# Kernel optimization log

Measured on AMD Instinct MI355X. Metric: run time of the kernel, lower is better.

Reference implementation:

```python
import jax, jax.numpy as jnp
import numpy as np
from jax import lax

NC = 8  # num_classes
NUM_ITERS = 2


def _resize_bilinear_ac(x, out_h, out_w):
    """Bilinear resize with align_corners=True, x: (N, C, H, W)."""
    N, C, H, W = x.shape

    def coords(n_out, n_in):
        if n_out == 1:
            return jnp.zeros((1,), jnp.float32)
        return jnp.linspace(0.0, float(n_in - 1), n_out, dtype=jnp.float32)

    ys = coords(out_h, H)
    xs = coords(out_w, W)
    y0 = jnp.floor(ys).astype(jnp.int32)
    y1 = jnp.minimum(y0 + 1, H - 1)
    wy = (ys - y0.astype(jnp.float32)).astype(x.dtype)
    x0 = jnp.floor(xs).astype(jnp.int32)
    x1 = jnp.minimum(x0 + 1, W - 1)
    wx = (xs - x0.astype(jnp.float32)).astype(x.dtype)

    r0 = x[:, :, y0, :]
    r1 = x[:, :, y1, :]
    r = r0 * (1.0 - wy)[None, None, :, None] + r1 * wy[None, None, :, None]
    c0 = r[:, :, :, x0]
    c1 = r[:, :, :, x1]
    return c0 * (1.0 - wx)[None, None, None, :] + c1 * wx[None, None, None, :]


def _conv2d(x, w, groups=1):
    k = w.shape[-1]
    pad = k // 2
    return lax.conv_general_dilated(
        x, w, window_strides=(1, 1), padding=[(pad, pad), (pad, pad)],
        dimension_numbers=('NCHW', 'OIHW', 'NCHW'), feature_group_count=groups)


def _mean_field_update(unary, guidance, spatial_w, bilateral_w, compat_w):
    Q = jax.nn.softmax(unary, axis=1)
    cw = compat_w[:, :, 0, 0]  # (O, I)
    for _ in range(NUM_ITERS):
        spatial_msg = _conv2d(Q, spatial_w, groups=NC)          # depthwise 3x3
        bilateral_in = jnp.concatenate([Q, guidance], axis=1)   # (N, NC+6, H, W)
        bilateral_msg = _conv2d(bilateral_in, bilateral_w)      # 3x3 dense
        message = spatial_msg + bilateral_msg
        message = jnp.einsum('nchw,oc->nohw', message, cw)      # 1x1 compat conv
        Q = jax.nn.softmax(unary - message, axis=1)
    return Q


def setup_inputs() -> dict:
    key = jax.random.key(0)
    ks = jax.random.split(key, 16)
    inp = {
        'logits': jax.random.normal(ks[0], (8, NC, 512, 512), jnp.float32),
        'image': jax.random.uniform(ks[1], (8, 3, 512, 512), jnp.float32),
        'skip0': jax.random.normal(ks[2], (8, 64, 256, 256), jnp.float32),
        'skip1': jax.random.normal(ks[3], (8, 128, 128, 128), jnp.float32),
        'skip2': jax.random.normal(ks[4], (8, 256, 64, 64), jnp.float32),
        'skip3': jax.random.normal(ks[5], (8, 512, 32, 32), jnp.float32),
        'spatial_w': jax.random.normal(ks[6], (NC, 1, 3, 3), jnp.float32) * 0.1,
        'bilateral_w': jax.random.normal(ks[7], (NC, NC + 6, 3, 3), jnp.float32) * 0.1,
        # compat_conv is initialized to -I (zeros then -= eye) in the module
        'compat_w': (-jnp.eye(NC, dtype=jnp.float32)).reshape(NC, NC, 1, 1),
        'skip_w0': jax.random.normal(ks[8], (3, 64, 1, 1), jnp.float32) * 0.05,
        'skip_b0': jnp.zeros((3,), jnp.float32),
        'skip_w1': jax.random.normal(ks[9], (3, 128, 1, 1), jnp.float32) * 0.05,
        'skip_b1': jnp.zeros((3,), jnp.float32),
        'skip_w2': jax.random.normal(ks[10], (3, 256, 1, 1), jnp.float32) * 0.05,
        'skip_b2': jnp.zeros((3,), jnp.float32),
        'skip_w3': jax.random.normal(ks[11], (3, 512, 1, 1), jnp.float32) * 0.05,
        'skip_b3': jnp.zeros((3,), jnp.float32),
    }
    return inp


def reference(logits, image, skip0, skip1, skip2, skip3,
              spatial_w, bilateral_w, compat_w,
              skip_w0, skip_b0, skip_w1, skip_b1,
              skip_w2, skip_b2, skip_w3, skip_b3):
    H, W = logits.shape[2], logits.shape[3]

    # fuse_skip_features: 1x1 project each skip to 3ch, upsample, average
    skips = [skip0, skip1, skip2, skip3]
    ws = [skip_w0, skip_w1, skip_w2, skip_w3]
    bs = [skip_b0, skip_b1, skip_b2, skip_b3]
    fused = jnp.zeros((logits.shape[0], 3, H, W), logits.dtype)
    for feat, w, b in zip(skips, ws, bs):
        p = jnp.einsum('nchw,oc->nohw', feat, w[:, :, 0, 0]) + b[None, :, None, None]
        fused = fused + _resize_bilinear_ac(p, H, W)
    fused = fused / len(skips)

    guidance = jnp.concatenate([image, fused], axis=1)  # (N, 6, H, W)

    Q_full = _mean_field_update(logits, guidance, spatial_w, bilateral_w, compat_w)

    logits_down = _resize_bilinear_ac(logits, H // 2, W // 2)
    guidance_down = _resize_bilinear_ac(guidance, H // 2, W // 2)
    Q_down = _mean_field_update(logits_down, guidance_down, spatial_w, bilateral_w, compat_w)
    Q_down_up = _resize_bilinear_ac(Q_down, H, W)

    return (Q_full + Q_down_up) / 2.0
```

## Files before the change

kernel.cpp:

```cpp
#include <hip/hip_runtime.h>
#include <hip/hip_fp16.h>
#include <math.h>

#define NB 8
#define NCLS 8
#define NGU 6
#define NBI 14
#define HF 512
#define WF 512
#define HH 256
#define WH 256

#define TOX 32
#define TOY 16
#define SX 36
#define SY 20
#define SPX (SY * SX)
#define R1W 36
#define R1N (18 * 36)
#define R1T 41
#define R2T 32
#define PLANE (SPX * 8)
#define PSTR (PLANE + 32)
#define TILEH (16 + PSTR + PLANE + 16)

typedef _Float16 f16x8 __attribute__((ext_vector_type(8)));
typedef float f32x4 __attribute__((ext_vector_type(4)));

static __device__ __forceinline__ void ac_prep(int o, float scale, int insz,
                                               int& i0, int& i1, float& f) {
    float s = (float)o * scale;
    int ii = (int)floorf(s);
    if (ii > insz - 1) ii = insz - 1;
    if (ii < 0) ii = 0;
    i0 = ii;
    i1 = (ii + 1 < insz) ? (ii + 1) : (insz - 1);
    f = s - (float)ii;
}

__global__ void k_fill_bias(float* __restrict__ out, const float* __restrict__ b, int HW) {
    int total = NB * 3 * HW;
    int idx = blockIdx.x * blockDim.x + threadIdx.x;
    if (idx >= total) return;
    int o = (idx / HW) % 3;
    out[idx] = b[o];
}

template <int VEC, bool DIRECT>
__global__ void k_skip_proj(const float* __restrict__ feat, const float* __restrict__ w,
                            const float* __restrict__ bias, float* __restrict__ out,
                            int C, int HW, int nch) {
    __shared__ float sw[3 * 512];
    for (int i = threadIdx.x; i < 3 * C; i += blockDim.x) sw[i] = w[i];
    __syncthreads();
    const int HWv = HW / VEC;
    int total = NB * HWv * nch;
    for (int idx = blockIdx.x * blockDim.x + threadIdx.x; idx < total;
         idx += gridDim.x * blockDim.x) {
        int hv = idx % HWv;
        int t = idx / HWv;
        int ch = t % nch;
        int n = t / nch;
        int c0 = ch * 64;
        const float* fp = feat + ((size_t)n * C + c0) * HW + (size_t)hv * VEC;
        float a[3][VEC];
        #pragma unroll
        for (int o = 0; o < 3; ++o)
            #pragma unroll
            for (int k = 0; k < VEC; ++k) a[o][k] = 0.f;
        #pragma unroll 4
        for (int c = 0; c < 64; ++c) {
            float v[VEC];
            if constexpr (VEC == 4) {
                float4 t4 = *reinterpret_cast<const float4*>(fp + (size_t)c * HW);
                v[0] = t4.x; v[1] = t4.y; v[2] = t4.z; v[3] = t4.w;
            } else if constexpr (VEC == 2) {
                float2 t2 = *reinterpret_cast<const float2*>(fp + (size_t)c * HW);
                v[0] = t2.x; v[1] = t2.y;
            } else {
                v[0] = fp[(size_t)c * HW];
            }
            #pragma unroll
            for (int o = 0; o < 3; ++o) {
                const float wv = sw[o * C + c0 + c];
                #pragma unroll
                for (int k = 0; k < VEC; ++k) a[o][k] = fmaf(wv, v[k], a[o][k]);
            }
        }
        float* op = out + (size_t)n * 3 * HW + (size_t)hv * VEC;
        #pragma unroll
        for (int o = 0; o < 3; ++o) {
            #pragma unroll
            for (int k = 0; k < VEC; ++k) {
                if (DIRECT)
                    op[(size_t)o * HW + k] = bias[o] + a[o][k];
                else
                    atomicAdd(&op[(size_t)o * HW + k], a[o][k]);
            }
        }
    }
}

__global__ void k_prep_full(const float* __restrict__ logits, const float* __restrict__ image,
                            const float* __restrict__ p0, const float* __restrict__ p1,
                            const float* __restrict__ p2, const float* __restrict__ p3,
                            _Float16* __restrict__ Gh, _Float16* __restrict__ Q0h) {
    const int HW = HF * WF;
    int idx = blockIdx.x * blockDim.x + threadIdx.x;
    if (idx >= NB * HW) return;
    int n = idx / HW, r = idx - n * HW;
    int y = r / WF, x = r - y * WF;

    const float* ps[4] = {p0, p1, p2, p3};
    const int ss[4] = {256, 128, 64, 32};
    float f[3] = {0.f, 0.f, 0.f};
    #pragma unroll
    for (int l = 0; l < 4; ++l) {
        int s = ss[l];
        float scale = (float)(s - 1) / 511.0f;
        int y0, y1, x0, x1;
        float fy, fx;
        ac_prep(y, scale, s, y0, y1, fy);
        ac_prep(x, scale, s, x0, x1, fx);
        const float* pb = ps[l] + (size_t)n * 3 * s * s;
        #pragma unroll
        for (int o = 0; o < 3; ++o) {
            const float* pp = pb + (size_t)o * s * s;
            float v00 = pp[y0 * s + x0], v01 = pp[y0 * s + x1];
            float v10 = pp[y1 * s + x0], v11 = pp[y1 * s + x1];
            float r0 = v00 * (1.f - fy) + v10 * fy;
            float r1 = v01 * (1.f - fy) + v11 * fy;
            f[o] += r0 * (1.f - fx) + r1 * fx;
        }
    }
    const float* ip = image + (size_t)n * 3 * HW + r;
    f16x8 gv;
    #pragma unroll
    for (int o = 0; o < 3; ++o) gv[o] = (_Float16)ip[(size_t)o * HW];
    #pragma unroll
    for (int o = 0; o < 3; ++o) gv[3 + o] = (_Float16)(f[o] * 0.25f);
    gv[6] = (_Float16)0.f;
    gv[7] = (_Float16)0.f;
    *(f16x8*)(Gh + (size_t)idx * 8) = gv;

    const float* up = logits + (size_t)n * NCLS * HW + r;
    float e[8];
    float s = 0.f;
    #pragma unroll
    for (int o = 0; o < 8; ++o) { e[o] = __expf(up[(size_t)o * HW]); s += e[o]; }
    float inv = 1.f / s;
    f16x8 qv;
    #pragma unroll
    for (int o = 0; o < 8; ++o) qv[o] = (_Float16)(e[o] * inv);
    *(f16x8*)(Q0h + (size_t)idx * 8) = qv;
}

__global__ void k_prep_w(const float* __restrict__ wsp, const float* __restrict__ wbil,
                         const float* __restrict__ cw, float* __restrict__ W2) {
    int i = blockIdx.x * blockDim.x + threadIdx.x;
    if (i >= NBI * 9 * 8) return;
    int o = i & 7;
    int t = (i >> 3) % 9;
    int ci = i / 72;
    float s = 0.f;
    for (int c = 0; c < NCLS; ++c)
        s += cw[o * NCLS + c] * wbil[((size_t)c * NBI + ci) * 9 + t];
    if (ci < NCLS) s += cw[o * NCLS + ci] * wsp[ci * 9 + t];
    W2[ci * 72 + t * 8 + o] = s;
}

__global__ void k_prep_frag(const float* __restrict__ W2, _Float16* __restrict__ wf) {
    int i = blockIdx.x * blockDim.x + threadIdx.x;
    if (i >= 5 * 64) return;
    int j = i >> 6, l = i & 63;
    int col = l & 15, kg = l >> 4;
    #pragma unroll
    for (int e = 0; e < 8; ++e) {
        int k = j * 32 + kg * 8 + e;
        int tap = k >> 4, ci = k & 15;
        float v = (tap < 9 && ci < 14 && col < 8) ? W2[ci * 72 + tap * 8 + col] : 0.f;
        wf[i * 8 + e] = (_Float16)v;
    }
}

template <bool DOWN, bool UPFOLD>
__global__ __launch_bounds__(256, 4) void k_mf_mfma(
    const float* __restrict__ unary, const _Float16* __restrict__ Q0h,
    const _Float16* __restrict__ Gh, const _Float16* __restrict__ Qd,
    void* __restrict__ QoutV, const _Float16* __restrict__ wfragG,
    int H, int W, int Hs, int Ws) {
    __shared__ __align__(16) _Float16 s_t[TILEH];
    __shared__ __align__(16) _Float16 s_msg[R1N * 8];
    _Float16* tb0 = s_t + 16;
    _Float16* tb1 = s_t + 16 + PSTR;

    const int tid = threadIdx.x;
    const int lane = tid & 63;
    const int wv = tid >> 6;
    const int n = blockIdx.z;
    const int gx0 = blockIdx.x * TOX;
    const int gy0 = blockIdx.y * TOY;
    const int HW = H * W;
    const int HWs = Hs * Ws;

    f16x8 wf[5];
    #pragma unroll
    for (int j = 0; j < 5; ++j)
        wf[j] = *(const f16x8*)(wfragG + (j * 64 + lane) * 8);

    if (tid < 16) s_t[tid] = (_Float16)0.f;
    else if (tid < 48) s_t[5760 + tid] = (_Float16)0.f;
    else if (tid < 64) s_t[11520 + tid] = (_Float16)0.f;

    const float syc = DOWN ? (float)(Hs - 1) / (float)(H - 1) : 1.f;
    const float sxc = DOWN ? (float)(Ws - 1) / (float)(W - 1) : 1.f;
    for (int i = tid; i < SPX; i += 256) {
        int yy = i / SX, xx = i - yy * SX;
        int gy = gy0 + yy - 2, gx = gx0 + xx - 2;
        f16x8 qv, gv;
        #pragma unroll
        for (int o = 0; o < 8; ++o) { qv[o] = (_Float16)0.f; gv[o] = (_Float16)0.f; }
        if ((unsigned)gy < (unsigned)H && (unsigned)gx < (unsigned)W) {
            if (DOWN) {
                int y0, y1, x0, x1;
                float fy, fx;
                ac_prep(gy, syc, Hs, y0, y1, fy);
                ac_prep(gx, sxc, Ws, x0, x1, fx);
                const float w00 = (1.f - fy) * (1.f - fx), w01 = (1.f - fy) * fx;
                const float w10 = fy * (1.f - fx), w11 = fy * fx;
                const size_t o00 = (size_t)y0 * Ws + x0, o01 = (size_t)y0 * Ws + x1;
                const size_t o10 = (size_t)y1 * Ws + x0, o11 = (size_t)y1 * Ws + x1;
                const float* ubase = unary + (size_t)n * NCLS * HWs;
                float e[8];
                float s = 0.f;
                #pragma unroll
                for (int o = 0; o < 8; ++o) {
                    const float* up = ubase + (size_t)o * HWs;
                    float u = w00 * up[o00] + w01 * up[o01] + w10 * up[o10] + w11 * up[o11];
                    e[o] = __expf(u);
                    s += e[o];
                }
                float inv = 1.f / s;
                #pragma unroll
                for (int o = 0; o < 8; ++o) qv[o] = (_Float16)(e[o] * inv);
                const size_t gb = (size_t)n * HWs;
                f16x8 ga = *(const f16x8*)(Gh + (gb + o00) * 8);
                f16x8 gb2 = *(const f16x8*)(Gh + (gb + o01) * 8);
                f16x8 gc = *(const f16x8*)(Gh + (gb + o10) * 8);
                f16x8 gd = *(const f16x8*)(Gh + (gb + o11) * 8);
                #pragma unroll
                for (int c = 0; c < 8; ++c) {
                    float g = w00 * (float)ga[c] + w01 * (float)gb2[c] +
                              w10 * (float)gc[c] + w11 * (float)gd[c];
                    gv[c] = (_Float16)g;
                }
            } else {
                const size_t off = ((size_t)n * HW + (size_t)gy * W + gx) * 8;
                qv = *(const f16x8*)(Q0h + off);
                gv = *(const f16x8*)(Gh + off);
            }
        }
        *(f16x8*)(tb0 + i * 8) = qv;
        *(f16x8*)(tb1 + i * 8) = gv;
    }
    __syncthreads();

    for (int t = wv; t < R1T; t += 4) {
        int pb = t * 16;
        int p = pb + (lane & 15);
        if (p > R1N - 1) p = R1N - 1;
        int qy = p / R1W;
        int yy = 1 + qy, xx = p - qy * R1W;
        int kg = lane >> 4;
        f32x4 acc = {0.f, 0.f, 0.f, 0.f};
        #pragma unroll
        for (int j = 0; j < 5; ++j) {
            int tap = 2 * j + (kg >> 1);
            if (tap > 8) tap = 8;
            int dy = tap / 3 - 1, dx = tap - (tap / 3) * 3 - 1;
            int idx = (yy + dy) * SX + (xx + dx);
            f16x8 af = *(const f16x8*)(tb0 + (kg & 1) * PSTR + idx * 8);
            acc = __builtin_amdgcn_mfma_f32_16x16x32_f16(af, wf[j], acc, 0, 0, 0);
        }
        int ch = lane & 15;
        if (ch < 8) {
            int pxb = pb + (lane >> 4) * 4;
            #pragma unroll
            for (int r = 0; r < 4; ++r) {
                int px = pxb + r;
                if (px < R1N) s_msg[px * 8 + ch] = (_Float16)acc[r];
            }
        }
    }
    __syncthreads();

    for (int i = tid; i < R1N; i += 256) {
        int qy = i / R1W;
        int yy = 1 + qy, xx = i - qy * R1W;
        int gy = gy0 + yy - 2, gx = gx0 + xx - 2;
        if ((unsigned)gy < (unsigned)H && (unsigned)gx < (unsigned)W) {
            f16x8 m = *(const f16x8*)(s_msg + i * 8);
            f16x8 q0 = *(const f16x8*)(tb0 + (i + SX) * 8);
            float e[8];
            float s = 0.f;
            #pragma unroll
            for (int o = 0; o < 8; ++o) {
                e[o] = (float)q0[o] * __expf(-(float)m[o]);
                s += e[o];
            }
            float inv = 1.f / s;
            f16x8 q1;
            #pragma unroll
            for (int o = 0; o < 8; ++o) q1[o] = (_Float16)(e[o] * inv);
            *(f16x8*)(tb0 + (i + SX) * 8) = q1;
        }
    }
    f16x8 m1r[2];
    #pragma unroll
    for (int u2 = 0; u2 < 2; ++u2) {
        int i = tid + 256 * u2;
        int oy = i >> 5, ox = i & 31;
        int r1 = (1 + oy) * R1W + (2 + ox);
        m1r[u2] = *(const f16x8*)(s_msg + r1 * 8);
    }
    __syncthreads();

    for (int t = wv; t < R2T; t += 4) {
        int pb = t * 16;
        int p = pb + (lane & 15);
        int yy = 2 + (p >> 5), xx = 2 + (p & 31);
        int kg = lane >> 4;
        f32x4 acc = {0.f, 0.f, 0.f, 0.f};
        #pragma unroll
        for (int j = 0; j < 5; ++j) {
            int tap = 2 * j + (kg >> 1);
            if (tap > 8) tap = 8;
            int dy = tap / 3 - 1, dx = tap - (tap / 3) * 3 - 1;
            int idx = (yy + dy) * SX + (xx + dx);
            f16x8 af = *(const f16x8*)(tb0 + (kg & 1) * PSTR + idx * 8);
            acc = __builtin_amdgcn_mfma_f32_16x16x32_f16(af, wf[j], acc, 0, 0, 0);
        }
        int ch = lane & 15;
        if (ch < 8) {
            int pxb = pb + (lane >> 4) * 4;
            #pragma unroll
            for (int r = 0; r < 4; ++r) s_msg[(pxb + r) * 8 + ch] = (_Float16)acc[r];
        }
    }
    __syncthreads();

    #pragma unroll
    for (int u2 = 0; u2 < 2; ++u2) {
        int i = tid + 256 * u2;
        int oy = i >> 5, ox = i & 31;
        int gy = gy0 + oy, gx = gx0 + ox;
        f16x8 m2 = *(const f16x8*)(s_msg + i * 8);
        f16x8 q1 = *(const f16x8*)(tb0 + ((2 + oy) * SX + (2 + ox)) * 8);
        float e[8];
        float s = 0.f;
        #pragma unroll
        for (int o = 0; o < 8; ++o) {
            e[o] = (float)q1[o] * __expf((float)m1r[u2][o] - (float)m2[o]);
            s += e[o];
        }
        float inv = 1.f / s;
        if (UPFOLD) {
            float* qp = (float*)QoutV + (size_t)n * NCLS * HW + (size_t)gy * W + gx;
            int y0, y1, x0, x1;
            float fy, fx;
            ac_prep(gy, 255.f / 511.f, HH, y0, y1, fy);
            ac_prep(gx, 255.f / 511.f, WH, x0, x1, fx);
            const float w00 = (1.f - fy) * (1.f - fx), w01 = (1.f - fy) * fx;
            const float w10 = fy * (1.f - fx), w11 = fy * fx;
            const size_t qb = (size_t)n * (HH * WH);
            f16x8 qa = *(const f16x8*)(Qd + (qb + (size_t)y0 * WH + x0) * 8);
            f16x8 qbv = *(const f16x8*)(Qd + (qb + (size_t)y0 * WH + x1) * 8);
            f16x8 qc = *(const f16x8*)(Qd + (qb + (size_t)y1 * WH + x0) * 8);
            f16x8 qdv = *(const f16x8*)(Qd + (qb + (size_t)y1 * WH + x1) * 8);
            #pragma unroll
            for (int o = 0; o < 8; ++o) {
                float v = w00 * (float)qa[o] + w01 * (float)qbv[o] +
                          w10 * (float)qc[o] + w11 * (float)qdv[o];
                qp[(size_t)o * HW] = fmaf(0.5f, e[o] * inv, 0.5f * v);
            }
        } else {
            _Float16* qo = (_Float16*)QoutV + ((size_t)n * HW + (size_t)gy * W + gx) * 8;
            f16x8 q2;
            #pragma unroll
            for (int o = 0; o < 8; ++o) q2[o] = (_Float16)(e[o] * inv);
            *(f16x8*)qo = q2;
        }
    }
}

static inline int cdiv(int a, int b) { return (a + b - 1) / b; }

extern "C" void kernel_launch(void* const* d_in, const int* in_sizes, int n_in,
                              void* d_out, int out_size, void* d_ws, size_t ws_size,
                              hipStream_t stream) {
    const float* logits = (const float*)d_in[0];
    const float* image = (const float*)d_in[1];
    const float* skip0 = (const float*)d_in[2];
    const float* skip1 = (const float*)d_in[3];
    const float* skip2 = (const float*)d_in[4];
    const float* skip3 = (const float*)d_in[5];
    const float* spatial_w = (const float*)d_in[6];
    const float* bilateral_w = (const float*)d_in[7];
    const float* compat_w = (const float*)d_in[8];
    const float* skip_w0 = (const float*)d_in[9];
    const float* skip_b0 = (const float*)d_in[10];
    const float* skip_w1 = (const float*)d_in[11];
    const float* skip_b1 = (const float*)d_in[12];
    const float* skip_w2 = (const float*)d_in[13];
    const float* skip_b2 = (const float*)d_in[14];
    const float* skip_w3 = (const float*)d_in[15];
    const float* skip_b3 = (const float*)d_in[16];
    float* out = (float*)d_out;
    float* ws = (float*)d_ws;

    float* p0 = ws + 0;
    float* p1 = ws + 1572864;
    float* p2 = ws + 1966080;
    float* p3 = ws + 2064384;
    float* W2 = ws + 2100000;
    _Float16* wfrag = (_Float16*)(ws + 2110000);
    _Float16* Q0h = (_Float16*)(ws + 4194304);
    _Float16* Gh = (_Float16*)(ws + 12582912);
    _Float16* Qdh = (_Float16*)(ws + 20971520);

    const int HWf = HF * WF;

    k_prep_w<<<4, 256, 0, stream>>>(spatial_w, bilateral_w, compat_w, W2);
    k_prep_frag<<<2, 256, 0, stream>>>(W2, wfrag);

    k_fill_bias<<<cdiv(NB * 3 * 16384, 256), 256, 0, stream>>>(p1, skip_b1, 16384);
    k_fill_bias<<<cdiv(NB * 3 * 4096, 256), 256, 0, stream>>>(p2, skip_b2, 4096);
    k_fill_bias<<<cdiv(NB * 3 * 1024, 256), 256, 0, stream>>>(p3, skip_b3, 1024);

    k_skip_proj<4, true><<<cdiv(NB * 16384 * 1, 256), 256, 0, stream>>>(
        skip0, skip_w0, skip_b0, p0, 64, 65536, 1);
    k_skip_proj<4, false><<<cdiv(NB * 4096 * 2, 256), 256, 0, stream>>>(
        skip1, skip_w1, skip_b1, p1, 128, 16384, 2);
    k_skip_proj<2, false><<<cdiv(NB * 2048 * 4, 256), 256, 0, stream>>>(
        skip2, skip_w2, skip_b2, p2, 256, 4096, 4);
    k_skip_proj<1, false><<<cdiv(NB * 1024 * 8, 256), 256, 0, stream>>>(
        skip3, skip_w3, skip_b3, p3, 512, 1024, 8);

    k_prep_full<<<cdiv(NB * HWf, 256), 256, 0, stream>>>(logits, image, p0, p1, p2, p3, Gh, Q0h);

    {
        dim3 grid(WH / TOX, HH / TOY, NB);
        k_mf_mfma<true, false><<<grid, 256, 0, stream>>>(
            logits, nullptr, Gh, nullptr, (void*)Qdh, wfrag, HH, WH, HF, WF);
    }

    {
        dim3 grid(WF / TOX, HF / TOY, NB);
        k_mf_mfma<false, true><<<grid, 256, 0, stream>>>(
            nullptr, Q0h, Gh, Qdh, (void*)out, wfrag, HF, WF, HF, WF);
    }
}
```

Before: 230.6 us.

## Merge prep launches, vectorize prep_full by two pixels, DMA interior tiles to LDS

Merges the two weight-prep kernels into one single-block kernel and the three bias-fill kernels into one, cutting launch count. k_prep_full now handles two adjacent pixels per thread with float2 loads of image and logits. For interior tiles of the full-resolution mean-field kernel, the Q0/guidance halo is copied with global_load_lds DMA straight into shared memory, and the bounds check in the softmax step is skipped there. The DMA path relies on the halo rows mapping contiguously to LDS, and relies on the existing barrier to cover completion of the async loads.

```diff
diff --git a/kernel.cpp b/kernel.cpp
--- a/kernel.cpp
+++ b/kernel.cpp
@@ -38,12 +38,21 @@
     f = s - (float)ii;
 }
 
-__global__ void k_fill_bias(float* __restrict__ out, const float* __restrict__ b, int HW) {
-    int total = NB * 3 * HW;
-    int idx = blockIdx.x * blockDim.x + threadIdx.x;
-    if (idx >= total) return;
-    int o = (idx / HW) % 3;
-    out[idx] = b[o];
+static __device__ __forceinline__ void dma16(const _Float16* g, _Float16* l) {
+    __builtin_amdgcn_global_load_lds(
+        (const __attribute__((address_space(1))) void*)g,
+        (__attribute__((address_space(3))) void*)l, 16, 0, 0);
+}
+
+__global__ void k_fill3(float* __restrict__ p1, float* __restrict__ p2,
+                        float* __restrict__ p3, const float* __restrict__ b1,
+                        const float* __restrict__ b2, const float* __restrict__ b3) {
+    int i = blockIdx.x * blockDim.x + threadIdx.x;
+    if (i < NB * 3 * 16384) { p1[i] = b1[(i / 16384) % 3]; return; }
+    i -= NB * 3 * 16384;
+    if (i < NB * 3 * 4096) { p2[i] = b2[(i / 4096) % 3]; return; }
+    i -= NB * 3 * 4096;
+    if (i < NB * 3 * 1024) p3[i] = b3[(i / 1024) % 3];
 }
 
 template <int VEC, bool DIRECT>
@@ -106,80 +115,98 @@
                             const float* __restrict__ p2, const float* __restrict__ p3,
                             _Float16* __restrict__ Gh, _Float16* __restrict__ Q0h) {
     const int HW = HF * WF;
-    int idx = blockIdx.x * blockDim.x + threadIdx.x;
-    if (idx >= NB * HW) return;
+    int t = blockIdx.x * blockDim.x + threadIdx.x;
+    if (t >= NB * HW / 2) return;
+    int idx = t * 2;
     int n = idx / HW, r = idx - n * HW;
     int y = r / WF, x = r - y * WF;
 
     const float* ps[4] = {p0, p1, p2, p3};
     const int ss[4] = {256, 128, 64, 32};
-    float f[3] = {0.f, 0.f, 0.f};
+    float f[2][3] = {{0.f, 0.f, 0.f}, {0.f, 0.f, 0.f}};
     #pragma unroll
     for (int l = 0; l < 4; ++l) {
         int s = ss[l];
         float scale = (float)(s - 1) / 511.0f;
-        int y0, y1, x0, x1;
-        float fy, fx;
+        int y0, y1;
+        float fy;
         ac_prep(y, scale, s, y0, y1, fy);
-        ac_prep(x, scale, s, x0, x1, fx);
         const float* pb = ps[l] + (size_t)n * 3 * s * s;
         #pragma unroll
-        for (int o = 0; o < 3; ++o) {
-            const float* pp = pb + (size_t)o * s * s;
-            float v00 = pp[y0 * s + x0], v01 = pp[y0 * s + x1];
-            float v10 = pp[y1 * s + x0], v11 = pp[y1 * s + x1];
-            float r0 = v00 * (1.f - fy) + v10 * fy;
-            float r1 = v01 * (1.f - fy) + v11 * fy;
-            f[o] += r0 * (1.f - fx) + r1 * fx;
+        for (int k = 0; k < 2; ++k) {
+            int x0, x1;
+            float fx;
+            ac_prep(x + k, scale, s, x0, x1, fx);
+            #pragma unroll
+            for (int o = 0; o < 3; ++o) {
+                const float* pp = pb + (size_t)o * s * s;
+                float v00 = pp[y0 * s + x0], v01 = pp[y0 * s + x1];
+                float v10 = pp[y1 * s + x0], v11 = pp[y1 * s + x1];
+                float r0 = v00 * (1.f - fy) + v10 * fy;
+                float r1 = v01 * (1.f - fy) + v11 * fy;
+                f[k][o] += r0 * (1.f - fx) + r1 * fx;
+            }
         }
     }
     const float* ip = image + (size_t)n * 3 * HW + r;
-    f16x8 gv;
-    #pragma unroll
-    for (int o = 0; o < 3; ++o) gv[o] = (_Float16)ip[(size_t)o * HW];
-    #pragma unroll
-    for (int o = 0; o < 3; ++o) gv[3 + o] = (_Float16)(f[o] * 0.25f);
-    gv[6] = (_Float16)0.f;
-    gv[7] = (_Float16)0.f;
-    *(f16x8*)(Gh + (size_t)idx * 8) = gv;
-
+    float2 img[3];
+    #pragma unroll
+    for (int o = 0; o < 3; ++o) img[o] = *reinterpret_cast<const float2*>(&ip[(size_t)o * HW]);
     const float* up = logits + (size_t)n * NCLS * HW + r;
-    float e[8];
-    float s = 0.f;
-    #pragma unroll
-    for (int o = 0; o < 8; ++o) { e[o] = __expf(up[(size_t)o * HW]); s += e[o]; }
-    float inv = 1.f / s;
-    f16x8 qv;
-    #pragma unroll
-    for (int o = 0; o < 8; ++o) qv[o] = (_Float16)(e[o] * inv);
-    *(f16x8*)(Q0h + (size_t)idx * 8) = qv;
-}
-
-__global__ void k_prep_w(const float* __restrict__ wsp, const float* __restrict__ wbil,
-                         const float* __restrict__ cw, float* __restrict__ W2) {
-    int i = blockIdx.x * blockDim.x + threadIdx.x;
-    if (i >= NBI * 9 * 8) return;
-    int o = i & 7;
-    int t = (i >> 3) % 9;
-    int ci = i / 72;
-    float s = 0.f;
-    for (int c = 0; c < NCLS; ++c)
-        s += cw[o * NCLS + c] * wbil[((size_t)c * NBI + ci) * 9 + t];
-    if (ci < NCLS) s += cw[o * NCLS + ci] * wsp[ci * 9 + t];
-    W2[ci * 72 + t * 8 + o] = s;
-}
-
-__global__ void k_prep_frag(const float* __restrict__ W2, _Float16* __restrict__ wf) {
-    int i = blockIdx.x * blockDim.x + threadIdx.x;
-    if (i >= 5 * 64) return;
-    int j = i >> 6, l = i & 63;
-    int col = l & 15, kg = l >> 4;
-    #pragma unroll
-    for (int e = 0; e < 8; ++e) {
-        int k = j * 32 + kg * 8 + e;
-        int tap = k >> 4, ci = k & 15;
-        float v = (tap < 9 && ci < 14 && col < 8) ? W2[ci * 72 + tap * 8 + col] : 0.f;
-        wf[i * 8 + e] = (_Float16)v;
+    float2 u[8];
+    #pragma unroll
+    for (int o = 0; o < 8; ++o) u[o] = *reinterpret_cast<const float2*>(&up[(size_t)o * HW]);
+
+    f16x8 gv[2], qv[2];
+    #pragma unroll
+    for (int k = 0; k < 2; ++k) {
+        gv[k][0] = (_Float16)(k ? img[0].y : img[0].x);
+        gv[k][1] = (_Float16)(k ? img[1].y : img[1].x);
+        gv[k][2] = (_Float16)(k ? img[2].y : img[2].x);
+        gv[k][3] = (_Float16)(f[k][0] * 0.25f);
+        gv[k][4] = (_Float16)(f[k][1] * 0.25f);
+        gv[k][5] = (_Float16)(f[k][2] * 0.25f);
+        gv[k][6] = (_Float16)0.f;
+        gv[k][7] = (_Float16)0.f;
+        float e[8];
+        float s = 0.f;
+        #pragma unroll
+        for (int o = 0; o < 8; ++o) { e[o] = __expf(k ? u[o].y : u[o].x); s += e[o]; }
+        float inv = 1.f / s;
+        #pragma unroll
+        for (int o = 0; o < 8; ++o) qv[k][o] = (_Float16)(e[o] * inv);
+    }
+    *(f16x8*)(Gh + (size_t)idx * 8) = gv[0];
+    *(f16x8*)(Gh + (size_t)idx * 8 + 8) = gv[1];
+    *(f16x8*)(Q0h + (size_t)idx * 8) = qv[0];
+    *(f16x8*)(Q0h + (size_t)idx * 8 + 8) = qv[1];
+}
+
+__global__ void k_prep_wf(const float* __restrict__ wsp, const float* __restrict__ wbil,
+                          const float* __restrict__ cw, _Float16* __restrict__ wf) {
+    __shared__ float sW2[NBI * 72];
+    int tid = threadIdx.x;
+    if (tid < NBI * 72) {
+        int o = tid & 7;
+        int t = (tid >> 3) % 9;
+        int ci = tid / 72;
+        float s = 0.f;
+        for (int c = 0; c < NCLS; ++c)
+            s += cw[o * NCLS + c] * wbil[((size_t)c * NBI + ci) * 9 + t];
+        if (ci < NCLS) s += cw[o * NCLS + ci] * wsp[ci * 9 + t];
+        sW2[tid] = s;
+    }
+    __syncthreads();
+    if (tid < 5 * 64) {
+        int l = tid & 63;
+        int col = l & 15, kg = l >> 4;
+        #pragma unroll
+        for (int e = 0; e < 8; ++e) {
+            int k = (tid >> 6) * 32 + kg * 8 + e;
+            int tap = k >> 4, ci = k & 15;
+            float v = (tap < 9 && ci < 14 && col < 8) ? sW2[ci * 72 + tap * 8 + col] : 0.f;
+            wf[tid * 8 + e] = (_Float16)v;
+        }
     }
 }
 
@@ -212,56 +239,72 @@
     else if (tid < 48) s_t[5760 + tid] = (_Float16)0.f;
     else if (tid < 64) s_t[11520 + tid] = (_Float16)0.f;
 
-    const float syc = DOWN ? (float)(Hs - 1) / (float)(H - 1) : 1.f;
-    const float sxc = DOWN ? (float)(Ws - 1) / (float)(W - 1) : 1.f;
-    for (int i = tid; i < SPX; i += 256) {
-        int yy = i / SX, xx = i - yy * SX;
-        int gy = gy0 + yy - 2, gx = gx0 + xx - 2;
-        f16x8 qv, gv;
-        #pragma unroll
-        for (int o = 0; o < 8; ++o) { qv[o] = (_Float16)0.f; gv[o] = (_Float16)0.f; }
-        if ((unsigned)gy < (unsigned)H && (unsigned)gx < (unsigned)W) {
-            if (DOWN) {
-                int y0, y1, x0, x1;
-                float fy, fx;
-                ac_prep(gy, syc, Hs, y0, y1, fy);
-                ac_prep(gx, sxc, Ws, x0, x1, fx);
-                const float w00 = (1.f - fy) * (1.f - fx), w01 = (1.f - fy) * fx;
-                const float w10 = fy * (1.f - fx), w11 = fy * fx;
-                const size_t o00 = (size_t)y0 * Ws + x0, o01 = (size_t)y0 * Ws + x1;
-                const size_t o10 = (size_t)y1 * Ws + x0, o11 = (size_t)y1 * Ws + x1;
-                const float* ubase = unary + (size_t)n * NCLS * HWs;
-                float e[8];
-                float s = 0.f;
-                #pragma unroll
-                for (int o = 0; o < 8; ++o) {
-                    const float* up = ubase + (size_t)o * HWs;
-                    float u = w00 * up[o00] + w01 * up[o01] + w10 * up[o10] + w11 * up[o11];
-                    e[o] = __expf(u);
-                    s += e[o];
+    const bool interior = !DOWN && gx0 >= 2 && (gx0 + TOX + 2) <= W &&
+                          gy0 >= 2 && (gy0 + TOY + 2) <= H;
+
+    if (!DOWN && interior) {
+        const size_t nb = (size_t)n * HW;
+        for (int c = wv; c < 12; c += 4) {
+            int px = c * 64 + lane;
+            int yy = px / SX, xx = px - yy * SX;
+            size_t goff = (nb + (size_t)(gy0 + yy - 2) * W + (gx0 + xx - 2)) * 8;
+            if (px < SPX) {
+                dma16(Q0h + goff, tb0 + (size_t)c * 64 * 8);
+                dma16(Gh + goff, tb1 + (size_t)c * 64 * 8);
+            }
+        }
+    } else {
+        const float syc = DOWN ? (float)(Hs - 1) / (float)(H - 1) : 1.f;
+        const float sxc = DOWN ? (float)(Ws - 1) / (float)(W - 1) : 1.f;
+        for (int i = tid; i < SPX; i += 256) {
+            int yy = i / SX, xx = i - yy * SX;
+            int gy = gy0 + yy - 2, gx = gx0 + xx - 2;
+            f16x8 qv, gv;
+            #pragma unroll
+            for (int o = 0; o < 8; ++o) { qv[o] = (_Float16)0.f; gv[o] = (_Float16)0.f; }
+            if ((unsigned)gy < (unsigned)H && (unsigned)gx < (unsigned)W) {
+                if (DOWN) {
+                    int y0, y1, x0, x1;
+                    float fy, fx;
+                    ac_prep(gy, syc, Hs, y0, y1, fy);
+                    ac_prep(gx, sxc, Ws, x0, x1, fx);
+                    const float w00 = (1.f - fy) * (1.f - fx), w01 = (1.f - fy) * fx;
+                    const float w10 = fy * (1.f - fx), w11 = fy * fx;
+                    const size_t o00 = (size_t)y0 * Ws + x0, o01 = (size_t)y0 * Ws + x1;
+                    const size_t o10 = (size_t)y1 * Ws + x0, o11 = (size_t)y1 * Ws + x1;
+                    const float* ubase = unary + (size_t)n * NCLS * HWs;
+                    float e[8];
+                    float s = 0.f;
+                    #pragma unroll
+                    for (int o = 0; o < 8; ++o) {
+                        const float* up = ubase + (size_t)o * HWs;
+                        float u = w00 * up[o00] + w01 * up[o01] + w10 * up[o10] + w11 * up[o11];
+                        e[o] = __expf(u);
+                        s += e[o];
+                    }
+                    float inv = 1.f / s;
+                    #pragma unroll
+                    for (int o = 0; o < 8; ++o) qv[o] = (_Float16)(e[o] * inv);
+                    const size_t gb = (size_t)n * HWs;
+                    f16x8 ga = *(const f16x8*)(Gh + (gb + o00) * 8);
+                    f16x8 gb2 = *(const f16x8*)(Gh + (gb + o01) * 8);
+                    f16x8 gc = *(const f16x8*)(Gh + (gb + o10) * 8);
+                    f16x8 gd = *(const f16x8*)(Gh + (gb + o11) * 8);
+                    #pragma unroll
+                    for (int c = 0; c < 8; ++c) {
+                        float g = w00 * (float)ga[c] + w01 * (float)gb2[c] +
+                                  w10 * (float)gc[c] + w11 * (float)gd[c];
+                        gv[c] = (_Float16)g;
+                    }
+                } else {
+                    const size_t off = ((size_t)n * HW + (size_t)gy * W + gx) * 8;
+                    qv = *(const f16x8*)(Q0h + off);
+                    gv = *(const f16x8*)(Gh + off);
                 }
-                float inv = 1.f / s;
-                #pragma unroll
-                for (int o = 0; o < 8; ++o) qv[o] = (_Float16)(e[o] * inv);
-                const size_t gb = (size_t)n * HWs;
-                f16x8 ga = *(const f16x8*)(Gh + (gb + o00) * 8);
-                f16x8 gb2 = *(const f16x8*)(Gh + (gb + o01) * 8);
-                f16x8 gc = *(const f16x8*)(Gh + (gb + o10) * 8);
-                f16x8 gd = *(const f16x8*)(Gh + (gb + o11) * 8);
-                #pragma unroll
-                for (int c = 0; c < 8; ++c) {
-                    float g = w00 * (float)ga[c] + w01 * (float)gb2[c] +
-                              w10 * (float)gc[c] + w11 * (float)gd[c];
-                    gv[c] = (_Float16)g;
-                }
-            } else {
-                const size_t off = ((size_t)n * HW + (size_t)gy * W + gx) * 8;
-                qv = *(const f16x8*)(Q0h + off);
-                gv = *(const f16x8*)(Gh + off);
-            }
-        }
-        *(f16x8*)(tb0 + i * 8) = qv;
-        *(f16x8*)(tb1 + i * 8) = gv;
+            }
+            *(f16x8*)(tb0 + i * 8) = qv;
+            *(f16x8*)(tb1 + i * 8) = gv;
+        }
     }
     __syncthreads();
 
@@ -298,7 +341,7 @@
         int qy = i / R1W;
         int yy = 1 + qy, xx = i - qy * R1W;
         int gy = gy0 + yy - 2, gx = gx0 + xx - 2;
-        if ((unsigned)gy < (unsigned)H && (unsigned)gx < (unsigned)W) {
+        if (interior || ((unsigned)gy < (unsigned)H && (unsigned)gx < (unsigned)W)) {
             f16x8 m = *(const f16x8*)(s_msg + i * 8);
             f16x8 q0 = *(const f16x8*)(tb0 + (i + SX) * 8);
             float e[8];
@@ -422,7 +465,6 @@
     float* p1 = ws + 1572864;
     float* p2 = ws + 1966080;
     float* p3 = ws + 2064384;
-    float* W2 = ws + 2100000;
     _Float16* wfrag = (_Float16*)(ws + 2110000);
     _Float16* Q0h = (_Float16*)(ws + 4194304);
     _Float16* Gh = (_Float16*)(ws + 12582912);
@@ -430,12 +472,10 @@
 
     const int HWf = HF * WF;
 
-    k_prep_w<<<4, 256, 0, stream>>>(spatial_w, bilateral_w, compat_w, W2);
-    k_prep_frag<<<2, 256, 0, stream>>>(W2, wfrag);
-
-    k_fill_bias<<<cdiv(NB * 3 * 16384, 256), 256, 0, stream>>>(p1, skip_b1, 16384);
-    k_fill_bias<<<cdiv(NB * 3 * 4096, 256), 256, 0, stream>>>(p2, skip_b2, 4096);
-    k_fill_bias<<<cdiv(NB * 3 * 1024, 256), 256, 0, stream>>>(p3, skip_b3, 1024);
+    k_prep_wf<<<1, 1024, 0, stream>>>(spatial_w, bilateral_w, compat_w, wfrag);
+
+    k_fill3<<<cdiv(NB * 3 * (16384 + 4096 + 1024), 256), 256, 0, stream>>>(
+        p1, p2, p3, skip_b1, skip_b2, skip_b3);
 
     k_skip_proj<4, true><<<cdiv(NB * 16384 * 1, 256), 256, 0, stream>>>(
         skip0, skip_w0, skip_b0, p0, 64, 65536, 1);
@@ -446,7 +486,8 @@
     k_skip_proj<1, false><<<cdiv(NB * 1024 * 8, 256), 256, 0, stream>>>(
         skip3, skip_w3, skip_b3, p3, 512, 1024, 8);
 
-    k_prep_full<<<cdiv(NB * HWf, 256), 256, 0, stream>>>(logits, image, p0, p1, p2, p3, Gh, Q0h);
+    k_prep_full<<<cdiv(NB * HWf / 2, 256), 256, 0, stream>>>(
+        logits, image, p0, p1, p2, p3, Gh, Q0h);
 
     {
         dim3 grid(WH / TOX, HH / TOY, NB);
```

New measurement: 226.7 us. Within noise of the previous version (-1.7%).
